# Optimization experiments

Hardware: AMD Instinct MI355X
Metric: run time of the kernel (lower is better)

## Reference

```python
import jax, jax.numpy as jnp
import numpy as np

TAU = 2.0  # self.temperature
EPS = 1e-7


def setup_inputs() -> dict:
    key = jax.random.key(0)
    kx, km, kw, kb, kc, kg = jax.random.split(key, 6)
    B, S, H = 8, 2048, 512
    G, V, D = 2, 320, 256  # num_groups, num_vars, codevector_dim
    hidden_states = jax.random.normal(kx, (B, S, H), dtype=jnp.float32)
    mask_time_indices = jax.random.randint(km, (B, S), 0, 2) > 0
    # nn.Linear(H, G*V)
    lim = 1.0 / np.sqrt(H)
    W_proj = jax.random.uniform(kw, (H, G * V), minval=-lim, maxval=lim, dtype=jnp.float32)
    b_proj = jax.random.uniform(kb, (G * V,), minval=-lim, maxval=lim, dtype=jnp.float32)
    codevectors = jax.random.normal(kc, (1, G * V, D // G), dtype=jnp.float32)
    # precomputed gumbel noise for determinism (torch samples inside gumbel_softmax)
    gumbels = jax.random.gumbel(kg, (B * S * G, V), dtype=jnp.float32)
    return {
        "hidden_states": hidden_states,
        "mask_time_indices": mask_time_indices,
        "W_proj": W_proj,
        "b_proj": b_proj,
        "codevectors": codevectors,
        "gumbels": gumbels,
    }


def reference(hidden_states, mask_time_indices, W_proj, b_proj, codevectors, gumbels):
    B, S, H = hidden_states.shape
    GV = W_proj.shape[1]
    V = gumbels.shape[-1]
    G = GV // V
    N = B * S

    logits = hidden_states @ W_proj + b_proj              # [B,S,G*V]
    flat = logits.reshape(N * G, V).astype(jnp.float32)    # [N*G, V]

    # gumbel_softmax(tau=TAU, hard=True) with straight-through estimator
    y_soft = jax.nn.softmax((flat + gumbels) / TAU, axis=-1)
    y_hard = jax.nn.one_hot(jnp.argmax(y_soft, axis=-1), V, dtype=y_soft.dtype)
    probs = y_hard + y_soft - jax.lax.stop_gradient(y_soft)  # [N*G, V]

    # perplexity from the (non-gumbel) soft distribution, masked marginals
    soft_dist = jax.nn.softmax(flat.reshape(N, G, V), axis=-1)
    m = mask_time_indices.reshape(-1).astype(soft_dist.dtype)  # [N]
    marginal = jnp.einsum('ngv,n->gv', soft_dist, m) / jnp.sum(m)
    perplexity = jnp.exp(-jnp.sum(marginal * jnp.log(marginal + EPS), axis=-1)).sum()

    # codebook combine: grouped one-hot mixture (avoids [N, G*V, D/G] blowup)
    cb = codevectors.reshape(G, V, -1)                     # [G, V, D/G]
    codevecs = jnp.einsum('ngv,gvd->ngd', probs.reshape(N, G, V), cb)
    codevecs = codevecs.reshape(B, S, -1)                  # [B, S, D]
    return codevecs, perplexity
```

## Files before the change

### kernel.cpp

```cpp
#include <hip/hip_runtime.h>
#include <hip/hip_bf16.h>
#include <math.h>

constexpr int Mn = 16384;
constexpr int Kd = 512;
constexpr int GV = 640;
constexpr int Vn = 320;
constexpr int Gn = 2;
constexpr int DG = 128;
constexpr float EPSc = 1e-7f;

constexpr int K2 = 1536;
constexpr int KA = 1024;
constexpr int NT = K2 / 32;

typedef _Float16 half8 __attribute__((ext_vector_type(8)));
typedef _Float16 half4 __attribute__((ext_vector_type(4)));
typedef float floatx4 __attribute__((ext_vector_type(4)));

#define WAITV(N) asm volatile("s_waitcnt vmcnt(" #N ")" ::: "memory")

__global__ __launch_bounds__(256) void convert_all(const float* __restrict__ h,
                                                   const float* __restrict__ W,
                                                   _Float16* __restrict__ A2,
                                                   _Float16* __restrict__ B2T,
                                                   float* __restrict__ marg) {
  const int bid = blockIdx.x;
  if (bid < 2048) {
    const int total = Mn * Kd / 4;
    for (int idx = bid * 256 + threadIdx.x; idx < total; idx += 2048 * 256) {
      float4 x = reinterpret_cast<const float4*>(h)[idx];
      int m = idx >> 7;
      int c = (idx & 127) << 2;
      half4 h0, h1;
      float xs[4] = {x.x, x.y, x.z, x.w};
#pragma unroll
      for (int j = 0; j < 4; ++j) {
        _Float16 a = (_Float16)xs[j];
        h0[j] = a;
        h1[j] = (_Float16)(xs[j] - (float)a);
      }
      *reinterpret_cast<half4*>(&A2[(size_t)m * KA + c]) = h0;
      *reinterpret_cast<half4*>(&A2[(size_t)m * KA + Kd + c]) = h1;
    }
  } else if (bid < 2208) {
    const int b2 = bid - 2048;
    const int wave = threadIdx.x >> 6, lane = threadIdx.x & 63;
    const int n = b2 * 4 + wave;
    _Float16* row = B2T + (size_t)n * K2;
#pragma unroll
    for (int j = 0; j < 8; ++j) {
      const int k = lane + 64 * j;
      const float w = W[(size_t)k * GV + n];
      const _Float16 w0 = (_Float16)w;
      const _Float16 w1 = (_Float16)(w - (float)w0);
      row[k] = w0;
      row[Kd + k] = w0;
      row[2 * Kd + k] = w1;
    }
  } else {
    for (int i = threadIdx.x; i <= GV; i += 256) marg[i] = 0.f;
  }
}

__global__ __launch_bounds__(256) void gemm_f16x2(const _Float16* __restrict__ A2,
                                                  const _Float16* __restrict__ B2T,
                                                  const float* __restrict__ bias,
                                                  float* __restrict__ C) {
  __shared__ _Float16 As[3 * 128 * 32];
  __shared__ _Float16 Bs[3 * 128 * 32];

  const int bid = blockIdx.x;
  const int sw = (bid & 7) * 80 + (bid >> 3);
  const int mt = sw / 5, nt = sw % 5;
  const int m0 = mt * 128, n0 = nt * 128;

  const int t = threadIdx.x, wv = t >> 6, l = t & 63;
  const int wr = wv >> 1, wc = wv & 1;
  const int lr = l & 15, lk = l >> 4;

  floatx4 acc[4][4] = {};

  auto stage = [&](int buf, int kt) {
    const int k2 = kt * 32;
    const int kA = k2 >= KA ? k2 - KA : k2;
    _Float16* abase = &As[buf * 4096];
    _Float16* bbase = &Bs[buf * 4096];
#pragma unroll
    for (int i = 0; i < 2; ++i) {
      const int idx = i * 256 + t;
      const int r = idx >> 2, s2 = idx & 3;
      const int sp = s2 ^ ((r >> 1) & 3);
      const _Float16* ga = A2 + (size_t)(m0 + r) * KA + kA + sp * 8;
      _Float16* la = abase + (i * 256 + wv * 64) * 8;
      __builtin_amdgcn_global_load_lds((const __attribute__((address_space(1))) void*)ga,
                                       (__attribute__((address_space(3))) void*)la, 16, 0, 0);
    }
#pragma unroll
    for (int i = 0; i < 2; ++i) {
      const int idx = i * 256 + t;
      const int r = idx >> 2, s2 = idx & 3;
      const int sp = s2 ^ ((r >> 1) & 3);
      const _Float16* gb = B2T + (size_t)(n0 + r) * K2 + k2 + sp * 8;
      _Float16* lb = bbase + (i * 256 + wv * 64) * 8;
      __builtin_amdgcn_global_load_lds((const __attribute__((address_space(1))) void*)gb,
                                       (__attribute__((address_space(3))) void*)lb, 16, 0, 0);
    }
  };

  stage(0, 0);
  stage(1, 1);

  int rb = 0, sb = 2;
  for (int kt = 0; kt < NT; ++kt) {
    if (kt < NT - 1) { WAITV(4); } else { WAITV(0); }
    __builtin_amdgcn_s_barrier();
    __builtin_amdgcn_sched_barrier(0);

    const _Float16* abase = &As[rb * 4096];
    const _Float16* bbase = &Bs[rb * 4096];
    half8 af[4], bf[4];
#pragma unroll
    for (int mi = 0; mi < 4; ++mi) {
      const int row = wr * 64 + mi * 16 + lr;
      const int sp = lk ^ ((row >> 1) & 3);
      af[mi] = *reinterpret_cast<const half8*>(&abase[row * 32 + sp * 8]);
    }
#pragma unroll
    for (int ni = 0; ni < 4; ++ni) {
      const int row = wc * 64 + ni * 16 + lr;
      const int sp = lk ^ ((row >> 1) & 3);
      bf[ni] = *reinterpret_cast<const half8*>(&bbase[row * 32 + sp * 8]);
    }

    if (kt + 2 < NT) stage(sb, kt + 2);

    __builtin_amdgcn_s_setprio(1);
#pragma unroll
    for (int mi = 0; mi < 4; ++mi)
#pragma unroll
      for (int ni = 0; ni < 4; ++ni)
        acc[mi][ni] = __builtin_amdgcn_mfma_f32_16x16x32_f16(af[mi], bf[ni], acc[mi][ni], 0, 0, 0);
    __builtin_amdgcn_s_setprio(0);

    rb = (rb == 2) ? 0 : rb + 1;
    sb = (sb == 2) ? 0 : sb + 1;
  }

#pragma unroll
  for (int ni = 0; ni < 4; ++ni) {
    const int gcol = n0 + wc * 64 + ni * 16 + lr;
    const float bv = bias[gcol];
#pragma unroll
    for (int mi = 0; mi < 4; ++mi) {
      const int grow = m0 + wr * 64 + mi * 16 + lk * 4;
#pragma unroll
      for (int j = 0; j < 4; ++j)
        C[(size_t)(grow + j) * GV + gcol] = acc[mi][ni][j] + bv;
    }
  }
}

__global__ __launch_bounds__(256) void row_kernel(const float* __restrict__ logits,
                                                  const float* __restrict__ gumbels,
                                                  const int* __restrict__ mask,
                                                  const float* __restrict__ codevectors,
                                                  float* __restrict__ out,
                                                  float* __restrict__ part,
                                                  float* __restrict__ marg) {
  __shared__ float lmarg[GV];
  const int wave = threadIdx.x >> 6, lane = threadIdx.x & 63;
  const int g = wave & 1;
  const int stream = wave >> 1;
  const int nbase = blockIdx.x * 8 + stream * 4;

  if (threadIdx.x < 8) {
    const int mk = (mask[blockIdx.x * 8 + threadIdx.x] != 0) ? 1 : 0;
    const unsigned long long b = __ballot(mk);
    if (threadIdx.x == 0) atomicAdd(&marg[GV], (float)__popcll(b & 0xFFull));
  }

  float acc[5] = {0.f, 0.f, 0.f, 0.f, 0.f};

  for (int it = 0; it < 2; ++it) {
    const int na = nbase + it * 2, nb = na + 1;
    const float* lrA = logits + (size_t)na * GV + g * Vn;
    const float* grA = gumbels + ((size_t)na * Gn + g) * Vn;
    const float* lrB = logits + (size_t)nb * GV + g * Vn;
    const float* grB = gumbels + ((size_t)nb * Gn + g) * Vn;

    float4 lA = reinterpret_cast<const float4*>(lrA)[lane];
    float4 gA = reinterpret_cast<const float4*>(grA)[lane];
    float lsA = lrA[256 + lane], gsA = grA[256 + lane];
    float4 lB = reinterpret_cast<const float4*>(lrB)[lane];
    float4 gB = reinterpret_cast<const float4*>(grB)[lane];
    float lsB = lrB[256 + lane], gsB = grB[256 + lane];

    float vA[5] = {lA.x, lA.y, lA.z, lA.w, lsA};
    float yA[5] = {lA.x + gA.x, lA.y + gA.y, lA.z + gA.z, lA.w + gA.w, lsA + gsA};
    float vB[5] = {lB.x, lB.y, lB.z, lB.w, lsB};
    float yB[5] = {lB.x + gB.x, lB.y + gB.y, lB.z + gB.z, lB.w + gB.w, lsB + gsB};

    float amA = yA[0], amB = yB[0];
    int aiA = lane * 4, aiB = lane * 4;
#pragma unroll
    for (int j = 1; j < 5; ++j) {
      const int v = (j < 4) ? lane * 4 + j : 256 + lane;
      if (yA[j] > amA) { amA = yA[j]; aiA = v; }
      if (yB[j] > amB) { amB = yB[j]; aiB = v; }
    }
#pragma unroll
    for (int off = 32; off; off >>= 1) {
      const float oA = __shfl_xor(amA, off);
      const int iA = __shfl_xor(aiA, off);
      if (oA > amA || (oA == amA && iA < aiA)) { amA = oA; aiA = iA; }
      const float oB = __shfl_xor(amB, off);
      const int iB = __shfl_xor(aiB, off);
      if (oB > amB || (oB == amB && iB < aiB)) { amB = oB; aiB = iB; }
    }

    float eA[5], eB[5], sA = 0.f, sB = 0.f;
#pragma unroll
    for (int j = 0; j < 5; ++j) {
      eA[j] = expf(vA[j]); sA += eA[j];
      eB[j] = expf(vB[j]); sB += eB[j];
    }
#pragma unroll
    for (int off = 32; off; off >>= 1) {
      sA += __shfl_xor(sA, off);
      sB += __shfl_xor(sB, off);
    }
    const float invA = 1.0f / sA, invB = 1.0f / sB;

    if (mask[na] != 0) {
#pragma unroll
      for (int j = 0; j < 5; ++j) acc[j] += eA[j] * invA;
    }
    if (mask[nb] != 0) {
#pragma unroll
      for (int j = 0; j < 5; ++j) acc[j] += eB[j] * invB;
    }

    const float* cvA = codevectors + ((size_t)g * Vn + aiA) * DG;
    float* orA = out + (size_t)na * (Gn * DG) + g * DG;
    orA[lane] = cvA[lane];
    orA[lane + 64] = cvA[lane + 64];
    const float* cvB = codevectors + ((size_t)g * Vn + aiB) * DG;
    float* orB = out + (size_t)nb * (Gn * DG) + g * DG;
    orB[lane] = cvB[lane];
    orB[lane + 64] = cvB[lane + 64];
  }

  if (stream == 0) {
#pragma unroll
    for (int j = 0; j < 4; ++j) lmarg[g * Vn + lane * 4 + j] = acc[j];
    lmarg[g * Vn + 256 + lane] = acc[4];
  }
  __syncthreads();
  if (stream == 1) {
#pragma unroll
    for (int j = 0; j < 4; ++j) lmarg[g * Vn + lane * 4 + j] += acc[j];
    lmarg[g * Vn + 256 + lane] += acc[4];
  }
  __syncthreads();
  float* prow = part + (size_t)blockIdx.x * GV;
  for (int i = threadIdx.x; i < GV; i += 256) prow[i] = lmarg[i];
}

__global__ __launch_bounds__(64) void reduce_marg(const float* __restrict__ part,
                                                  float* __restrict__ marg) {
  const int c = blockIdx.x * 64 + threadIdx.x;
  const int r0 = blockIdx.y * 64;
  float s = 0.f;
#pragma unroll 8
  for (int r = 0; r < 64; ++r) s += part[(size_t)(r0 + r) * GV + c];
  atomicAdd(&marg[c], s);
}

__global__ __launch_bounds__(640) void finalize(const float* __restrict__ marg,
                                                float* __restrict__ out_pp) {
  __shared__ float wred[10];
  const int t = threadIdx.x, wave = t >> 6, lane = t & 63;
  const float msum = marg[GV];

  const float p = marg[t] / msum;
  float e = p * logf(p + EPSc);
#pragma unroll
  for (int off = 32; off; off >>= 1) e += __shfl_xor(e, off);
  if (lane == 0) wred[wave] = e;
  __syncthreads();
  if (t == 0) {
    const float e0 = wred[0] + wred[1] + wred[2] + wred[3] + wred[4];
    const float e1 = wred[5] + wred[6] + wred[7] + wred[8] + wred[9];
    out_pp[0] = expf(-e0) + expf(-e1);
  }
}

extern "C" void kernel_launch(void* const* d_in, const int* in_sizes, int n_in,
                              void* d_out, int out_size, void* d_ws, size_t ws_size,
                              hipStream_t stream) {
  const float* hidden      = (const float*)d_in[0];
  const int*   mask        = (const int*)d_in[1];
  const float* W           = (const float*)d_in[2];
  const float* bias        = (const float*)d_in[3];
  const float* codevectors = (const float*)d_in[4];
  const float* gumbels     = (const float*)d_in[5];
  float* out = (float*)d_out;

  const size_t cBytes  = (size_t)Mn * GV * sizeof(float);
  const size_t a2Off   = cBytes + 8192;
  const size_t a2Bytes = (size_t)Mn * KA * sizeof(_Float16);
  const size_t b2tOff  = a2Off + a2Bytes;

  float*    logits = (float*)d_ws;
  float*    marg   = (float*)((char*)d_ws + cBytes);
  _Float16* A2     = (_Float16*)((char*)d_ws + a2Off);
  _Float16* B2T    = (_Float16*)((char*)d_ws + b2tOff);
  float*    part   = (float*)A2;

  convert_all<<<2209, 256, 0, stream>>>(hidden, W, A2, B2T, marg);
  gemm_f16x2<<<640, 256, 0, stream>>>(A2, B2T, bias, logits);
  row_kernel<<<Mn / 8, 256, 0, stream>>>(logits, gumbels, mask, codevectors, out, part, marg);
  reduce_marg<<<dim3(10, 32), 64, 0, stream>>>(part, marg);
  finalize<<<1, 640, 0, stream>>>(marg, out + (size_t)Mn * (Gn * DG));
}
```

Baseline: 108.6 us.

## Split row kernel into stats and codevector gather kernels, drop LDS marginal merge

The fused row kernel is split in two. One kernel computes the softmax statistics and argmax indices, writing the indices to a workspace array and per-stream partial marginals straight to global memory with no shared-memory merge or block barriers. A separate gather kernel then copies the selected codevectors with float4 loads and stores. The intent is to shorten the main kernel and vectorise the output copy. The cost is one extra launch, an index round trip through global memory, and twice as many partial rows for reduce_marg to sum.

```diff
diff --git a/kernel.cpp b/kernel.cpp
--- a/kernel.cpp
+++ b/kernel.cpp
@@ -161,14 +161,12 @@
   }
 }
 
-__global__ __launch_bounds__(256) void row_kernel(const float* __restrict__ logits,
-                                                  const float* __restrict__ gumbels,
-                                                  const int* __restrict__ mask,
-                                                  const float* __restrict__ codevectors,
-                                                  float* __restrict__ out,
-                                                  float* __restrict__ part,
-                                                  float* __restrict__ marg) {
-  __shared__ float lmarg[GV];
+__global__ __launch_bounds__(256) void stats_kernel(const float* __restrict__ logits,
+                                                    const float* __restrict__ gumbels,
+                                                    const int* __restrict__ mask,
+                                                    int* __restrict__ idxArr,
+                                                    float* __restrict__ part,
+                                                    float* __restrict__ marg) {
   const int wave = threadIdx.x >> 6, lane = threadIdx.x & 63;
   const int g = wave & 1;
   const int stream = wave >> 1;
@@ -241,30 +239,33 @@
       for (int j = 0; j < 5; ++j) acc[j] += eB[j] * invB;
     }
 
-    const float* cvA = codevectors + ((size_t)g * Vn + aiA) * DG;
-    float* orA = out + (size_t)na * (Gn * DG) + g * DG;
-    orA[lane] = cvA[lane];
-    orA[lane + 64] = cvA[lane + 64];
-    const float* cvB = codevectors + ((size_t)g * Vn + aiB) * DG;
-    float* orB = out + (size_t)nb * (Gn * DG) + g * DG;
-    orB[lane] = cvB[lane];
-    orB[lane + 64] = cvB[lane + 64];
-  }
-
-  if (stream == 0) {
-#pragma unroll
-    for (int j = 0; j < 4; ++j) lmarg[g * Vn + lane * 4 + j] = acc[j];
-    lmarg[g * Vn + 256 + lane] = acc[4];
-  }
-  __syncthreads();
-  if (stream == 1) {
-#pragma unroll
-    for (int j = 0; j < 4; ++j) lmarg[g * Vn + lane * 4 + j] += acc[j];
-    lmarg[g * Vn + 256 + lane] += acc[4];
-  }
-  __syncthreads();
-  float* prow = part + (size_t)blockIdx.x * GV;
-  for (int i = threadIdx.x; i < GV; i += 256) prow[i] = lmarg[i];
+    if (lane == 0) {
+      idxArr[na * Gn + g] = aiA;
+      idxArr[nb * Gn + g] = aiB;
+    }
+  }
+
+  float* prow = part + (size_t)(blockIdx.x * 2 + stream) * GV + g * Vn;
+  float4 a4 = {acc[0], acc[1], acc[2], acc[3]};
+  *reinterpret_cast<float4*>(&prow[lane * 4]) = a4;
+  prow[256 + lane] = acc[4];
+}
+
+__global__ __launch_bounds__(256) void gather_kernel(const int* __restrict__ idxArr,
+                                                     const float* __restrict__ codevectors,
+                                                     float* __restrict__ out) {
+  const int t = threadIdx.x;
+  const int r = t >> 5, q = t & 31;
+  const int n = blockIdx.x * 8 + r;
+  const int g = q >> 4;
+  const int d = (q * 8) & 127;
+  const int i = idxArr[n * Gn + g];
+  const float* cv = codevectors + ((size_t)(g * Vn + i)) * DG + d;
+  float4 a = *reinterpret_cast<const float4*>(cv);
+  float4 b = *reinterpret_cast<const float4*>(cv + 4);
+  float* o = out + (size_t)n * (Gn * DG) + g * DG + d;
+  *reinterpret_cast<float4*>(o) = a;
+  *reinterpret_cast<float4*>(o + 4) = b;
 }
 
 __global__ __launch_bounds__(64) void reduce_marg(const float* __restrict__ part,
@@ -317,10 +318,12 @@
   _Float16* A2     = (_Float16*)((char*)d_ws + a2Off);
   _Float16* B2T    = (_Float16*)((char*)d_ws + b2tOff);
   float*    part   = (float*)A2;
+  int*      idxArr = (int*)((char*)d_ws + a2Off + (16u << 20));
 
   convert_all<<<2209, 256, 0, stream>>>(hidden, W, A2, B2T, marg);
   gemm_f16x2<<<640, 256, 0, stream>>>(A2, B2T, bias, logits);
-  row_kernel<<<Mn / 8, 256, 0, stream>>>(logits, gumbels, mask, codevectors, out, part, marg);
-  reduce_marg<<<dim3(10, 32), 64, 0, stream>>>(part, marg);
+  stats_kernel<<<Mn / 8, 256, 0, stream>>>(logits, gumbels, mask, idxArr, part, marg);
+  gather_kernel<<<Mn / 8, 256, 0, stream>>>(idxArr, codevectors, out);
+  reduce_marg<<<dim3(10, 64), 64, 0, stream>>>(part, marg);
   finalize<<<1, 640, 0, stream>>>(marg, out + (size_t)Mn * (Gn * DG));
 }
```

Result: slower. 115.2 us (+6.1%).
